# Performance work log

Measured on AMD Instinct MI355X. Metric: run time of the kernel, lower is better.

The kernel has to match this reference:

```python
import jax, jax.numpy as jnp
import numpy as np

DEPTH = 6            # full octree depth (64^3 effective resolution)
DATA_DIM = 28        # 9*3 SH coeffs + 1 density -> sh_order = 2
SH_ORDER = 2
B_RAYS = 32768
MAX_STEPS = 192      # max DDA cell crossings for a 64^3 grid
STEP_SIZE = 0.001
BG_BRIGHTNESS = 1.0

SH_C0 = 0.28209479177387814
SH_C1 = 0.4886025119029199
SH_C2 = (1.0925484305920792, -1.0925484305920792, 0.31539156525252005,
         -1.0925484305920792, 0.5462742152960396)


def _build_full_tree_child():
    # Full octree in BFS order; child stores relative offsets, 0 = leaf.
    n_nodes = (8 ** DEPTH - 1) // 7
    child = np.zeros((n_nodes, 2, 2, 2), np.int32)
    off = 0
    for d in range(DEPTH - 1):
        cnt = 8 ** d
        nxt = off + cnt
        r = np.arange(cnt)
        j = nxt + r[:, None] * 8 + np.arange(8)[None, :]
        child[off:nxt] = (j - (off + r)[:, None]).reshape(cnt, 2, 2, 2)
        off = nxt
    return child


def setup_inputs() -> dict:
    key = jax.random.key(0)
    k0, k1, k2, k3 = jax.random.split(key, 4)
    n_nodes = (8 ** DEPTH - 1) // 7
    data = jax.random.normal(k0, (n_nodes, 2, 2, 2, DATA_DIM), jnp.float32)
    child = jnp.asarray(_build_full_tree_child())
    origins = jax.random.normal(k1, (B_RAYS, 3), jnp.float32) * 0.3
    dirs = jax.random.normal(k2, (B_RAYS, 3), jnp.float32)
    vd = jax.random.normal(k3, (B_RAYS, 3), jnp.float32)
    viewdirs = vd / jnp.linalg.norm(vd, axis=-1, keepdims=True)
    offset = jnp.full((3,), 0.5, jnp.float32)
    invradius = jnp.full((1,), 0.5, jnp.float32)
    return dict(data=data, child=child, origins=origins, dirs=dirs,
                viewdirs=viewdirs, offset=offset, invradius=invradius)


def eval_sh_bases2(v):
    # svox sh.eval_sh_bases for order 2 -> (B, 9)
    x, y, z = v[:, 0], v[:, 1], v[:, 2]
    return jnp.stack([
        jnp.full_like(x, SH_C0),
        -SH_C1 * y, SH_C1 * z, -SH_C1 * x,
        SH_C2[0] * x * y, SH_C2[1] * y * z,
        SH_C2[2] * (2.0 * z * z - x * x - y * y),
        SH_C2[3] * x * z, SH_C2[4] * (x * x - y * y)], axis=-1)


def dda_unit(cen, invdir):
    # intersection of ray with the unit cube [0,1]^3; returns (tmin>=0, tmax)
    t1 = -cen * invdir
    t2 = t1 + invdir
    tmin = jnp.maximum(0.0, jnp.max(jnp.minimum(t1, t2), axis=-1))
    tmax = jnp.minimum(1e9, jnp.min(jnp.maximum(t1, t2), axis=-1))
    return tmin, tmax


def tree_query(data, child, pos):
    # Walk the octree from root; returns (leaf rgba (B,D), cell size (B,), cell corner (B,3))
    B = pos.shape[0]
    node = jnp.zeros((B,), jnp.int32)
    corner = jnp.zeros_like(pos)
    csz = jnp.ones((B,), pos.dtype)
    done = jnp.zeros((B,), bool)
    fin_node = node
    fin_idx = jnp.zeros((B, 3), jnp.int32)
    for _ in range(DEPTH):
        rel = (pos - corner) / csz[:, None]
        idx = jnp.clip(jnp.floor(rel * 2.0).astype(jnp.int32), 0, 1)
        c_cell = csz * 0.5
        corner_cell = corner + idx.astype(pos.dtype) * c_cell[:, None]
        ch = child[node, idx[:, 0], idx[:, 1], idx[:, 2]]
        leaf = ch == 0
        newly = (~done) & leaf
        fin_node = jnp.where(newly, node, fin_node)
        fin_idx = jnp.where(newly[:, None], idx, fin_idx)
        upd = ~done
        corner = jnp.where(upd[:, None], corner_cell, corner)
        csz = jnp.where(upd, c_cell, csz)
        node = jnp.where(upd & (~leaf), node + ch, node)
        done = done | leaf
    rgba = data[fin_node, fin_idx[:, 0], fin_idx[:, 1], fin_idx[:, 2]]
    return rgba, csz, corner


def _render(data, child, origins, dirs, viewdirs, offset, invradius):
    B = origins.shape[0]
    og = offset[None, :] + origins * invradius[0]          # world2tree
    d = dirs / jnp.linalg.norm(dirs, axis=-1, keepdims=True)
    invd = 1.0 / (d + 1e-9)
    t0, tmax = dda_unit(og, invd)
    sh_mult = eval_sh_bases2(viewdirs)                     # (B, 9)
    delta_scale = 1.0 / invradius[0]

    def body(carry, _):
        t, light, out, active = carry
        pos = og + t[:, None] * d
        rgba, csz, corner = tree_query(data, child, pos)
        pos_t = (pos - corner) / csz[:, None]
        tmn, tmx = dda_unit(pos_t, invd)
        dt = (tmx - tmn) * csz + STEP_SIZE
        att = jnp.exp(-dt * jax.nn.relu(rgba[:, -1]) * delta_scale)
        w = jnp.where(active, light * (1.0 - att), 0.0)
        rgb_sh = rgba[:, :-1].reshape(-1, 3, (SH_ORDER + 1) ** 2)
        rgb = jax.nn.sigmoid(jnp.sum(sh_mult[:, None, :] * rgb_sh, axis=-1))
        out = out + w[:, None] * rgb
        light = jnp.where(active, light * att, light)
        t = jnp.where(active, t + dt, t)
        active = active & (t < tmax)
        return (t, light, out, active), None

    init = (t0, jnp.ones((B,), og.dtype), jnp.zeros((B, 3), og.dtype), t0 < tmax)
    (t, light, out, active), _ = jax.lax.scan(body, init, None, length=MAX_STEPS)
    return out + BG_BRIGHTNESS * light[:, None]


_render_jit = jax.jit(_render)


def reference(data, child, origins, dirs, viewdirs, offset, invradius):
    return _render_jit(data, child, origins, dirs, viewdirs, offset, invradius)
```

## Files before the change

kernel.cpp:

```cpp
#include <hip/hip_runtime.h>
#include <hip/hip_fp16.h>
#include <math.h>

#pragma clang fp contract(off)


constexpr float STEP_SIZE  = 0.001f;
constexpr int   KC   = 16;
constexpr int   CH   = 12;
constexpr float SH_C0   = 0.28209479177387814f;
constexpr float SH_C1   = 0.4886025119029199f;
constexpr float SH_C2_0 = 1.0925484305920792f;
constexpr float SH_C2_1 = -1.0925484305920792f;
constexpr float SH_C2_2 = 0.31539156525252005f;
constexpr float SH_C2_3 = -1.0925484305920792f;
constexpr float SH_C2_4 = 0.5462742152960396f;
constexpr unsigned LEAF_BASE   = 37448u;
constexpr unsigned NLEAF       = 262144u;
constexpr unsigned LEAF_F32OFF = LEAF_BASE * 28u;
constexpr size_t   TABLE_BYTES = (size_t)NLEAF * 64;

__device__ __forceinline__ unsigned spread6(unsigned v) {
    v = (v | (v << 8)) & 0x0300F00Fu;
    v = (v | (v << 4)) & 0x030C30C3u;
    v = (v | (v << 2)) & 0x09249249u;
    return v;
}

__device__ __forceinline__ float2 h2f(unsigned u) {
    return __half22float2(__builtin_bit_cast(__half2, u));
}

__global__ void __launch_bounds__(256)
vr_convert(const float* __restrict__ data, __half2* __restrict__ o, int total)
{
    int tid = blockIdx.x * 256 + threadIdx.x;
    if (tid >= total) return;
    unsigned c = (unsigned)tid >> 4, j = (unsigned)tid & 15u;
    const float* src = data + LEAF_F32OFF + c * 28u;
    float a, b;
    if (j == 0u)      { a = src[27]; b = src[0]; }
    else if (j < 14u) { a = src[2 * j - 1]; b = src[2 * j]; }
    else              { a = 0.f; b = 0.f; }
    o[tid] = __float22half2_rn(make_float2(a, b));
}

#define RAY_SETUP                                                             \
    const float invr   = invradius[0];                                        \
    float ogx = offset[0] + origins[3 * ray + 0] * invr;                      \
    float ogy = offset[1] + origins[3 * ray + 1] * invr;                      \
    float ogz = offset[2] + origins[3 * ray + 2] * invr;                      \
    float Dx = dirs[3 * ray + 0], Dy = dirs[3 * ray + 1], Dz = dirs[3 * ray + 2]; \
    float dn = sqrtf(Dx * Dx + Dy * Dy + Dz * Dz);                            \
    float dx = Dx / dn, dy = Dy / dn, dz = Dz / dn;                           \
    float ivx = 1.0f / (dx + 1e-9f);                                          \
    float ivy = 1.0f / (dy + 1e-9f);                                          \
    float ivz = 1.0f / (dz + 1e-9f);                                          \
    float t1x = -ogx * ivx, t2x = t1x + ivx;                                  \
    float t1y = -ogy * ivy, t2y = t1y + ivy;                                  \
    float t1z = -ogz * ivz, t2z = t1z + ivz;                                  \
    float t    = fmaxf(0.f, fmaxf(fmaxf(fminf(t1x, t2x), fminf(t1y, t2y)),    \
                                  fminf(t1z, t2z)));                          \
    float tmax = fminf(1e9f, fminf(fminf(fmaxf(t1x, t2x), fmaxf(t1y, t2y)),   \
                                   fmaxf(t1z, t2z)));

#define GEO_BODY(OUT_DT, OUT_VOX)                                            \
    float px = ogx + t * dx;                                                 \
    float py = ogy + t * dy;                                                 \
    float pz = ogz + t * dz;                                                 \
    float fx = px * 64.f, fy = py * 64.f, fz = pz * 64.f;                    \
    float vxf = fminf(fmaxf(floorf(fx), 0.f), 63.f);                         \
    float vyf = fminf(fmaxf(floorf(fy), 0.f), 63.f);                         \
    float vzf = fminf(fmaxf(floorf(fz), 0.f), 63.f);                         \
    float ptx = fx - vxf, pty = fy - vyf, ptz = fz - vzf;                    \
    float b1x = -ptx * ivx, b2x = b1x + ivx;                                 \
    float b1y = -pty * ivy, b2y = b1y + ivy;                                 \
    float b1z = -ptz * ivz, b2z = b1z + ivz;                                 \
    float tmn = fmaxf(0.f, fmaxf(fmaxf(fminf(b1x, b2x), fminf(b1y, b2y)),    \
                                 fminf(b1z, b2z)));                          \
    float tmx = fminf(1e9f, fminf(fminf(fmaxf(b1x, b2x), fmaxf(b1y, b2y)),   \
                                  fmaxf(b1z, b2z)));                         \
    OUT_DT = (tmx - tmn) * 0.015625f + STEP_SIZE;                            \
    OUT_VOX = (spread6((unsigned)(int)vxf) << 2) |                           \
              (spread6((unsigned)(int)vyf) << 1) |                           \
               spread6((unsigned)(int)vzf);

__global__ void __launch_bounds__(64)
vr_tpass(const float* __restrict__ origins,
         const float* __restrict__ dirs,
         const float* __restrict__ offset,
         const float* __restrict__ invradius,
         float* __restrict__ tb, int nrays)
{
    int ray = blockIdx.x * 64 + threadIdx.x;
    if (ray >= nrays) return;
    RAY_SETUP
    bool act = t < tmax;
    for (int c = 0; c < KC; ++c) {
        tb[c * nrays + ray] = t;
        if (c == KC - 1) break;
        for (int s = 0; s < CH; ++s) {
            if (act) {
                float dtv; unsigned vox;
                GEO_BODY(dtv, vox)
                (void)vox;
                t += dtv;
                act = (t < tmax);
            }
        }
    }
}

__global__ void __launch_bounds__(64)
vr_march16(const uint4* __restrict__ table,
           const float* __restrict__ tb,
           const float* __restrict__ origins,
           const float* __restrict__ dirs,
           const float* __restrict__ viewdirs,
           const float* __restrict__ offset,
           const float* __restrict__ invradius,
           float4* __restrict__ ws4, int nrays)
{
    int ray = blockIdx.x * 64 + threadIdx.x;
    if (ray >= nrays) return;
    int chunk = blockIdx.y;

    RAY_SETUP
    const float dscale = 1.0f / invr;

    t = tb[chunk * nrays + ray];
    bool act = t < tmax;

    float lcl = 1.f, o0 = 0.f, o1 = 0.f, o2 = 0.f;

    if (__any(act)) {
        float vx_ = viewdirs[3 * ray + 0], vy_ = viewdirs[3 * ray + 1],
              vz_ = viewdirs[3 * ray + 2];
        float sh0 = SH_C0;
        float sh1 = -SH_C1 * vy_;
        float sh2 =  SH_C1 * vz_;
        float sh3 = -SH_C1 * vx_;
        float sh4 = SH_C2_0 * (vx_ * vy_);
        float sh5 = SH_C2_1 * (vy_ * vz_);
        float sh6 = SH_C2_2 * (2.f * (vz_ * vz_) - vx_ * vx_ - vy_ * vy_);
        float sh7 = SH_C2_3 * (vx_ * vz_);
        float sh8 = SH_C2_4 * (vx_ * vx_ - vy_ * vy_);

        for (int s = 0; s < CH; ++s) {
            if (!__any(act)) break;
            if (act) {
                float dtv; unsigned vox;
                GEO_BODY(dtv, vox)

                const uint4* tp = table + (size_t)vox * 4u;
                uint4 q0 = tp[0], q1 = tp[1], q2 = tp[2], q3 = tp[3];
                float2 F0 = h2f(q0.x);
                float sigma = F0.x;
                if (sigma > 0.f) {
                    float2 F1 = h2f(q0.y), F2 = h2f(q0.z), F3 = h2f(q0.w);
                    float2 F4 = h2f(q1.x), F5 = h2f(q1.y), F6 = h2f(q1.z), F7 = h2f(q1.w);
                    float2 F8 = h2f(q2.x), F9 = h2f(q2.y), F10 = h2f(q2.z), F11 = h2f(q2.w);
                    float2 F12 = h2f(q3.x), F13 = h2f(q3.y);

                    float d0 = fmaf(sh0, F0.y, fmaf(sh1, F1.x, fmaf(sh2, F1.y,
                               fmaf(sh3, F2.x, fmaf(sh4, F2.y, fmaf(sh5, F3.x,
                               fmaf(sh6, F3.y, fmaf(sh7, F4.x, sh8 * F4.y))))))));
                    float d1 = fmaf(sh0, F5.x, fmaf(sh1, F5.y, fmaf(sh2, F6.x,
                               fmaf(sh3, F6.y, fmaf(sh4, F7.x, fmaf(sh5, F7.y,
                               fmaf(sh6, F8.x, fmaf(sh7, F8.y, sh8 * F9.x))))))));
                    float d2 = fmaf(sh0, F9.y, fmaf(sh1, F10.x, fmaf(sh2, F10.y,
                               fmaf(sh3, F11.x, fmaf(sh4, F11.y, fmaf(sh5, F12.x,
                               fmaf(sh6, F12.y, fmaf(sh7, F13.x, sh8 * F13.y))))))));

                    float att = __expf(-dtv * sigma * dscale);
                    float w   = lcl * (1.f - att);
                    float s0  = __builtin_amdgcn_rcpf(1.f + __expf(-d0));
                    float s1  = __builtin_amdgcn_rcpf(1.f + __expf(-d1));
                    float s2  = __builtin_amdgcn_rcpf(1.f + __expf(-d2));
                    o0 = fmaf(w, s0, o0);
                    o1 = fmaf(w, s1, o1);
                    o2 = fmaf(w, s2, o2);
                    lcl *= att;
                }

                t += dtv;
                act = (t < tmax);
            }
        }
    }

    ws4[chunk * nrays + ray] = make_float4(o0, o1, o2, lcl);
}

__global__ void vr_march32(const float* __restrict__ data,
                           const float* __restrict__ origins,
                           const float* __restrict__ dirs,
                           const float* __restrict__ viewdirs,
                           const float* __restrict__ offset,
                           const float* __restrict__ invradius,
                           float4* __restrict__ ws4, int nrays)
{
    constexpr int CHS = 48;
    int ray = blockIdx.x * 64 + threadIdx.x;
    if (ray >= nrays) return;
    int chunk = blockIdx.y;

    RAY_SETUP
    const float dscale = 1.0f / invr;

    float vx_ = viewdirs[3 * ray + 0], vy_ = viewdirs[3 * ray + 1],
          vz_ = viewdirs[3 * ray + 2];
    float sh0 = SH_C0;
    float sh1 = -SH_C1 * vy_;
    float sh2 =  SH_C1 * vz_;
    float sh3 = -SH_C1 * vx_;
    float sh4 = SH_C2_0 * (vx_ * vy_);
    float sh5 = SH_C2_1 * (vy_ * vz_);
    float sh6 = SH_C2_2 * (2.f * (vz_ * vz_) - vx_ * vx_ - vy_ * vy_);
    float sh7 = SH_C2_3 * (vx_ * vz_);
    float sh8 = SH_C2_4 * (vx_ * vx_ - vy_ * vy_);

    float lcl = 1.f, o0 = 0.f, o1 = 0.f, o2 = 0.f;
    bool act = t < tmax;

    int warm = chunk * CHS;
    for (int s = 0; s < warm; ++s) {
        if (!__any(act)) break;
        if (act) {
            float dtv; unsigned vox;
            GEO_BODY(dtv, vox)
            (void)vox;
            t += dtv;
            act = (t < tmax);
        }
    }

    for (int s = 0; s < CHS; ++s) {
        if (!__any(act)) break;
        if (act) {
            float dtv; unsigned vox;
            GEO_BODY(dtv, vox)
            const float4* p = (const float4*)(data + (LEAF_BASE + vox) * 28u);
            float4 a0 = p[0], a1 = p[1], a2 = p[2], a3 = p[3],
                   a4 = p[4], a5 = p[5], a6 = p[6];
            float d0 = fmaf(sh0, a0.x, fmaf(sh1, a0.y, fmaf(sh2, a0.z,
                       fmaf(sh3, a0.w, fmaf(sh4, a1.x, fmaf(sh5, a1.y,
                       fmaf(sh6, a1.z, fmaf(sh7, a1.w, sh8 * a2.x))))))));
            float d1 = fmaf(sh0, a2.y, fmaf(sh1, a2.z, fmaf(sh2, a2.w,
                       fmaf(sh3, a3.x, fmaf(sh4, a3.y, fmaf(sh5, a3.z,
                       fmaf(sh6, a3.w, fmaf(sh7, a4.x, sh8 * a4.y))))))));
            float d2 = fmaf(sh0, a4.z, fmaf(sh1, a4.w, fmaf(sh2, a5.x,
                       fmaf(sh3, a5.y, fmaf(sh4, a5.z, fmaf(sh5, a5.w,
                       fmaf(sh6, a6.x, fmaf(sh7, a6.y, sh8 * a6.z))))))));
            float att = __expf(-dtv * fmaxf(a6.w, 0.f) * dscale);
            float w   = lcl * (1.f - att);
            float s0  = __builtin_amdgcn_rcpf(1.f + __expf(-d0));
            float s1  = __builtin_amdgcn_rcpf(1.f + __expf(-d1));
            float s2  = __builtin_amdgcn_rcpf(1.f + __expf(-d2));
            o0 = fmaf(w, s0, o0);
            o1 = fmaf(w, s1, o1);
            o2 = fmaf(w, s2, o2);
            lcl *= att;
            t += dtv;
            act = (t < tmax);
        }
    }

    ws4[chunk * nrays + ray] = make_float4(o0, o1, o2, lcl);
}

template<int K>
__global__ void __launch_bounds__(256)
vr_combine(const float4* __restrict__ ws4, float* __restrict__ out, int nrays)
{
    int r = blockIdx.x * 256 + threadIdx.x;
    if (r >= nrays) return;
    float4 c = ws4[(K - 1) * nrays + r];
    float ax = c.x, ay = c.y, az = c.z, L = c.w;
#pragma unroll
    for (int cidx = K - 2; cidx >= 0; --cidx) {
        float4 p = ws4[cidx * nrays + r];
        ax = p.x + p.w * ax;
        ay = p.y + p.w * ay;
        az = p.z + p.w * az;
        L *= p.w;
    }
    out[3 * r + 0] = ax + L;
    out[3 * r + 1] = ay + L;
    out[3 * r + 2] = az + L;
}

extern "C" void kernel_launch(void* const* d_in, const int* in_sizes, int n_in,
                              void* d_out, int out_size, void* d_ws, size_t ws_size,
                              hipStream_t stream)
{
    const float* data      = (const float*)d_in[0];
    const float* origins   = (const float*)d_in[2];
    const float* dirs      = (const float*)d_in[3];
    const float* viewdirs  = (const float*)d_in[4];
    const float* offset    = (const float*)d_in[5];
    const float* invradius = (const float*)d_in[6];
    float* out = (float*)d_out;

    int nrays = in_sizes[2] / 3;
    size_t tb_bytes   = (size_t)KC * nrays * sizeof(float);
    size_t part_bytes = (size_t)KC * nrays * sizeof(float4);
    dim3 gridC((nrays + 255) / 256), blockC(256);

    if (ws_size >= TABLE_BYTES + tb_bytes + part_bytes) {
        __half2* table_h2 = (__half2*)d_ws;
        float*   tb       = (float*)((char*)d_ws + TABLE_BYTES);
        float4*  ws4      = (float4*)((char*)d_ws + TABLE_BYTES + tb_bytes);

        int total = (int)(NLEAF * 16u);
        dim3 gridV((total + 255) / 256), blockV(256);
        hipLaunchKernelGGL(vr_convert, gridV, blockV, 0, stream,
                           data, table_h2, total);

        dim3 gridT((nrays + 63) / 64), blockT(64);
        hipLaunchKernelGGL(vr_tpass, gridT, blockT, 0, stream,
                           origins, dirs, offset, invradius, tb, nrays);

        dim3 gridM((nrays + 63) / 64, KC), blockM(64);
        hipLaunchKernelGGL(vr_march16, gridM, blockM, 0, stream,
                           (const uint4*)d_ws, tb, origins, dirs, viewdirs,
                           offset, invradius, ws4, nrays);

        hipLaunchKernelGGL((vr_combine<KC>), gridC, blockC, 0, stream,
                           ws4, out, nrays);
    } else {
        float4* ws4 = (float4*)d_ws;
        dim3 gridM((nrays + 63) / 64, 4), blockM(64);
        hipLaunchKernelGGL(vr_march32, gridM, blockM, 0, stream,
                           data, origins, dirs, viewdirs,
                           offset, invradius, ws4, nrays);
        hipLaunchKernelGGL((vr_combine<4>), gridC, blockC, 0, stream,
                           ws4, out, nrays);
    }
}
```

Before: 57.34 us.

## Split leaf table into sigma/color halves, batch lookups, drop t-pass kernel

The fp16 leaf table is split into an 8-byte part holding sigma plus the first coefficients and a 48-byte part holding the rest of the color data. The march kernel now prefetches the small part for batches of 8 steps before shading, and loads the large part only when sigma is positive. The separate t-pass kernel is removed: each chunk re-marches its warm-up steps itself, with fewer, longer chunks (8x24 instead of 16x12). This trades repeated geometry work in later chunks for one less launch and one less global buffer, and aims to hide gather latency and skip color loads for empty cells.

```diff
diff --git a/kernel.cpp b/kernel.cpp
--- a/kernel.cpp
+++ b/kernel.cpp
@@ -6,8 +6,9 @@
 
 
 constexpr float STEP_SIZE  = 0.001f;
-constexpr int   KC   = 16;
-constexpr int   CH   = 12;
+constexpr int   KC   = 8;
+constexpr int   CH   = 24;
+constexpr int   SB   = 8;
 constexpr float SH_C0   = 0.28209479177387814f;
 constexpr float SH_C1   = 0.4886025119029199f;
 constexpr float SH_C2_0 = 1.0925484305920792f;
@@ -18,7 +19,8 @@
 constexpr unsigned LEAF_BASE   = 37448u;
 constexpr unsigned NLEAF       = 262144u;
 constexpr unsigned LEAF_F32OFF = LEAF_BASE * 28u;
-constexpr size_t   TABLE_BYTES = (size_t)NLEAF * 64;
+constexpr size_t   A_BYTES = (size_t)NLEAF * 8;
+constexpr size_t   B_BYTES = (size_t)NLEAF * 48;
 
 __device__ __forceinline__ unsigned spread6(unsigned v) {
     v = (v | (v << 8)) & 0x0300F00Fu;
@@ -30,19 +32,27 @@
 __device__ __forceinline__ float2 h2f(unsigned u) {
     return __half22float2(__builtin_bit_cast(__half2, u));
 }
+__device__ __forceinline__ unsigned f2h2(float a, float b) {
+    return __builtin_bit_cast(unsigned, __float22half2_rn(make_float2(a, b)));
+}
 
 __global__ void __launch_bounds__(256)
-vr_convert(const float* __restrict__ data, __half2* __restrict__ o, int total)
-{
-    int tid = blockIdx.x * 256 + threadIdx.x;
-    if (tid >= total) return;
-    unsigned c = (unsigned)tid >> 4, j = (unsigned)tid & 15u;
-    const float* src = data + LEAF_F32OFF + c * 28u;
-    float a, b;
-    if (j == 0u)      { a = src[27]; b = src[0]; }
-    else if (j < 14u) { a = src[2 * j - 1]; b = src[2 * j]; }
-    else              { a = 0.f; b = 0.f; }
-    o[tid] = __float22half2_rn(make_float2(a, b));
+vr_convert(const float* __restrict__ data,
+           uint2* __restrict__ tabA, uint4* __restrict__ tabB)
+{
+    unsigned leaf = blockIdx.x * 256 + threadIdx.x;
+    if (leaf >= NLEAF) return;
+    const float4* sp = (const float4*)(data + LEAF_F32OFF + leaf * 28u);
+    float4 a0 = sp[0], a1 = sp[1], a2 = sp[2], a3 = sp[3],
+           a4 = sp[4], a5 = sp[5], a6 = sp[6];
+    tabA[leaf] = make_uint2(f2h2(a6.w, a0.x), f2h2(a0.y, a0.z));
+    uint4* bp = tabB + (size_t)leaf * 3u;
+    bp[0] = make_uint4(f2h2(a0.w, a1.x), f2h2(a1.y, a1.z),
+                       f2h2(a1.w, a2.x), f2h2(a2.y, a2.z));
+    bp[1] = make_uint4(f2h2(a2.w, a3.x), f2h2(a3.y, a3.z),
+                       f2h2(a3.w, a4.x), f2h2(a4.y, a4.z));
+    bp[2] = make_uint4(f2h2(a4.w, a5.x), f2h2(a5.y, a5.z),
+                       f2h2(a5.w, a6.x), f2h2(a6.y, a6.z));
 }
 
 #define RAY_SETUP                                                             \
@@ -63,6 +73,19 @@
                                   fminf(t1z, t2z)));                          \
     float tmax = fminf(1e9f, fminf(fminf(fmaxf(t1x, t2x), fmaxf(t1y, t2y)),   \
                                    fmaxf(t1z, t2z)));
+
+#define SH_SETUP                                                              \
+    float vx_ = viewdirs[3 * ray + 0], vy_ = viewdirs[3 * ray + 1],           \
+          vz_ = viewdirs[3 * ray + 2];                                        \
+    float sh0 = SH_C0;                                                        \
+    float sh1 = -SH_C1 * vy_;                                                 \
+    float sh2 =  SH_C1 * vz_;                                                 \
+    float sh3 = -SH_C1 * vx_;                                                 \
+    float sh4 = SH_C2_0 * (vx_ * vy_);                                        \
+    float sh5 = SH_C2_1 * (vy_ * vz_);                                        \
+    float sh6 = SH_C2_2 * (2.f * (vz_ * vz_) - vx_ * vx_ - vy_ * vy_);        \
+    float sh7 = SH_C2_3 * (vx_ * vz_);                                        \
+    float sh8 = SH_C2_4 * (vx_ * vx_ - vy_ * vy_);
 
 #define GEO_BODY(OUT_DT, OUT_VOX)                                            \
     float px = ogx + t * dx;                                                 \
@@ -85,94 +108,84 @@
               (spread6((unsigned)(int)vyf) << 1) |                           \
                spread6((unsigned)(int)vzf);
 
-__global__ void __launch_bounds__(64)
-vr_tpass(const float* __restrict__ origins,
-         const float* __restrict__ dirs,
-         const float* __restrict__ offset,
-         const float* __restrict__ invradius,
-         float* __restrict__ tb, int nrays)
+__global__ void vr_march16(const uint2* __restrict__ tabA,
+                           const uint4* __restrict__ tabB,
+                           const float* __restrict__ origins,
+                           const float* __restrict__ dirs,
+                           const float* __restrict__ viewdirs,
+                           const float* __restrict__ offset,
+                           const float* __restrict__ invradius,
+                           float4* __restrict__ ws4, int nrays)
 {
     int ray = blockIdx.x * 64 + threadIdx.x;
     if (ray >= nrays) return;
+    int chunk = blockIdx.y;
+
     RAY_SETUP
+    const float dscale = 1.0f / invr;
+    SH_SETUP
+
+    float lcl = 1.f, o0 = 0.f, o1 = 0.f, o2 = 0.f;
     bool act = t < tmax;
-    for (int c = 0; c < KC; ++c) {
-        tb[c * nrays + ray] = t;
-        if (c == KC - 1) break;
-        for (int s = 0; s < CH; ++s) {
+
+    int warm = chunk * CH;
+    for (int s = 0; s < warm; ++s) {
+        if (!__any(act)) break;
+        if (act) {
+            float dtv; unsigned vox;
+            GEO_BODY(dtv, vox)
+            (void)vox;
+            t += dtv;
+            act = (t < tmax);
+        }
+    }
+
+    for (int b = 0; b < CH / SB; ++b) {
+        if (!__any(act)) break;
+
+        float    dtA[SB];
+        unsigned voxA[SB];
+        uint2    qA[SB];
+        unsigned amask = 0u;
+
+#pragma unroll
+        for (int j = 0; j < SB; ++j) {
             if (act) {
                 float dtv; unsigned vox;
                 GEO_BODY(dtv, vox)
-                (void)vox;
+                dtA[j]  = dtv;
+                voxA[j] = vox;
+                qA[j]   = tabA[vox];
+                amask  |= (1u << j);
                 t += dtv;
                 act = (t < tmax);
             }
         }
-    }
-}
-
-__global__ void __launch_bounds__(64)
-vr_march16(const uint4* __restrict__ table,
-           const float* __restrict__ tb,
-           const float* __restrict__ origins,
-           const float* __restrict__ dirs,
-           const float* __restrict__ viewdirs,
-           const float* __restrict__ offset,
-           const float* __restrict__ invradius,
-           float4* __restrict__ ws4, int nrays)
-{
-    int ray = blockIdx.x * 64 + threadIdx.x;
-    if (ray >= nrays) return;
-    int chunk = blockIdx.y;
-
-    RAY_SETUP
-    const float dscale = 1.0f / invr;
-
-    t = tb[chunk * nrays + ray];
-    bool act = t < tmax;
-
-    float lcl = 1.f, o0 = 0.f, o1 = 0.f, o2 = 0.f;
-
-    if (__any(act)) {
-        float vx_ = viewdirs[3 * ray + 0], vy_ = viewdirs[3 * ray + 1],
-              vz_ = viewdirs[3 * ray + 2];
-        float sh0 = SH_C0;
-        float sh1 = -SH_C1 * vy_;
-        float sh2 =  SH_C1 * vz_;
-        float sh3 = -SH_C1 * vx_;
-        float sh4 = SH_C2_0 * (vx_ * vy_);
-        float sh5 = SH_C2_1 * (vy_ * vz_);
-        float sh6 = SH_C2_2 * (2.f * (vz_ * vz_) - vx_ * vx_ - vy_ * vy_);
-        float sh7 = SH_C2_3 * (vx_ * vz_);
-        float sh8 = SH_C2_4 * (vx_ * vx_ - vy_ * vy_);
-
-        for (int s = 0; s < CH; ++s) {
-            if (!__any(act)) break;
-            if (act) {
-                float dtv; unsigned vox;
-                GEO_BODY(dtv, vox)
-
-                const uint4* tp = table + (size_t)vox * 4u;
-                uint4 q0 = tp[0], q1 = tp[1], q2 = tp[2], q3 = tp[3];
-                float2 F0 = h2f(q0.x);
+
+#pragma unroll
+        for (int j = 0; j < SB; ++j) {
+            if ((amask >> j) & 1u) {
+                float2 F0 = h2f(qA[j].x);
                 float sigma = F0.x;
                 if (sigma > 0.f) {
-                    float2 F1 = h2f(q0.y), F2 = h2f(q0.z), F3 = h2f(q0.w);
-                    float2 F4 = h2f(q1.x), F5 = h2f(q1.y), F6 = h2f(q1.z), F7 = h2f(q1.w);
-                    float2 F8 = h2f(q2.x), F9 = h2f(q2.y), F10 = h2f(q2.z), F11 = h2f(q2.w);
-                    float2 F12 = h2f(q3.x), F13 = h2f(q3.y);
+                    float2 F1 = h2f(qA[j].y);
+                    const uint4* bp = tabB + (size_t)voxA[j] * 3u;
+                    uint4 B0 = bp[0], B1 = bp[1], B2 = bp[2];
+                    float2 G0 = h2f(B0.x), G1 = h2f(B0.y), G2 = h2f(B0.z), G3 = h2f(B0.w);
+                    float2 H0 = h2f(B1.x), H1 = h2f(B1.y), H2 = h2f(B1.z), H3 = h2f(B1.w);
+                    float2 I0 = h2f(B2.x), I1 = h2f(B2.y), I2 = h2f(B2.z), I3 = h2f(B2.w);
 
                     float d0 = fmaf(sh0, F0.y, fmaf(sh1, F1.x, fmaf(sh2, F1.y,
-                               fmaf(sh3, F2.x, fmaf(sh4, F2.y, fmaf(sh5, F3.x,
-                               fmaf(sh6, F3.y, fmaf(sh7, F4.x, sh8 * F4.y))))))));
-                    float d1 = fmaf(sh0, F5.x, fmaf(sh1, F5.y, fmaf(sh2, F6.x,
-                               fmaf(sh3, F6.y, fmaf(sh4, F7.x, fmaf(sh5, F7.y,
-                               fmaf(sh6, F8.x, fmaf(sh7, F8.y, sh8 * F9.x))))))));
-                    float d2 = fmaf(sh0, F9.y, fmaf(sh1, F10.x, fmaf(sh2, F10.y,
-                               fmaf(sh3, F11.x, fmaf(sh4, F11.y, fmaf(sh5, F12.x,
-                               fmaf(sh6, F12.y, fmaf(sh7, F13.x, sh8 * F13.y))))))));
-
-                    float att = __expf(-dtv * sigma * dscale);
+                               fmaf(sh3, G0.x, fmaf(sh4, G0.y, fmaf(sh5, G1.x,
+                               fmaf(sh6, G1.y, fmaf(sh7, G2.x, sh8 * G2.y))))))));
+                    float d1 = fmaf(sh0, G3.x, fmaf(sh1, G3.y, fmaf(sh2, H0.x,
+                               fmaf(sh3, H0.y, fmaf(sh4, H1.x, fmaf(sh5, H1.y,
+                               fmaf(sh6, H2.x, fmaf(sh7, H2.y, sh8 * H3.x))))))));
+                    float d2 = fmaf(sh0, H3.y, fmaf(sh1, I0.x, fmaf(sh2, I0.y,
+                               fmaf(sh3, I1.x, fmaf(sh4, I1.y, fmaf(sh5, I2.x,
+                               fmaf(sh6, I2.y, fmaf(sh7, I3.x, sh8 * I3.y))))))));
+
+                    float att = __expf(-dtA[j] * sigma * dscale);
                     float w   = lcl * (1.f - att);
                     float s0  = __builtin_amdgcn_rcpf(1.f + __expf(-d0));
                     float s1  = __builtin_amdgcn_rcpf(1.f + __expf(-d1));
@@ -182,9 +195,6 @@
                     o2 = fmaf(w, s2, o2);
                     lcl *= att;
                 }
-
-                t += dtv;
-                act = (t < tmax);
             }
         }
     }
@@ -207,18 +217,7 @@
 
     RAY_SETUP
     const float dscale = 1.0f / invr;
-
-    float vx_ = viewdirs[3 * ray + 0], vy_ = viewdirs[3 * ray + 1],
-          vz_ = viewdirs[3 * ray + 2];
-    float sh0 = SH_C0;
-    float sh1 = -SH_C1 * vy_;
-    float sh2 =  SH_C1 * vz_;
-    float sh3 = -SH_C1 * vx_;
-    float sh4 = SH_C2_0 * (vx_ * vy_);
-    float sh5 = SH_C2_1 * (vy_ * vz_);
-    float sh6 = SH_C2_2 * (2.f * (vz_ * vz_) - vx_ * vx_ - vy_ * vy_);
-    float sh7 = SH_C2_3 * (vx_ * vz_);
-    float sh8 = SH_C2_4 * (vx_ * vx_ - vy_ * vy_);
+    SH_SETUP
 
     float lcl = 1.f, o0 = 0.f, o1 = 0.f, o2 = 0.f;
     bool act = t < tmax;
@@ -303,27 +302,21 @@
     float* out = (float*)d_out;
 
     int nrays = in_sizes[2] / 3;
-    size_t tb_bytes   = (size_t)KC * nrays * sizeof(float);
     size_t part_bytes = (size_t)KC * nrays * sizeof(float4);
     dim3 gridC((nrays + 255) / 256), blockC(256);
 
-    if (ws_size >= TABLE_BYTES + tb_bytes + part_bytes) {
-        __half2* table_h2 = (__half2*)d_ws;
-        float*   tb       = (float*)((char*)d_ws + TABLE_BYTES);
-        float4*  ws4      = (float4*)((char*)d_ws + TABLE_BYTES + tb_bytes);
-
-        int total = (int)(NLEAF * 16u);
-        dim3 gridV((total + 255) / 256), blockV(256);
+    if (ws_size >= A_BYTES + B_BYTES + part_bytes) {
+        uint2*  tabA = (uint2*)d_ws;
+        uint4*  tabB = (uint4*)((char*)d_ws + A_BYTES);
+        float4* ws4  = (float4*)((char*)d_ws + A_BYTES + B_BYTES);
+
+        dim3 gridV((NLEAF + 255) / 256), blockV(256);
         hipLaunchKernelGGL(vr_convert, gridV, blockV, 0, stream,
-                           data, table_h2, total);
-
-        dim3 gridT((nrays + 63) / 64), blockT(64);
-        hipLaunchKernelGGL(vr_tpass, gridT, blockT, 0, stream,
-                           origins, dirs, offset, invradius, tb, nrays);
+                           data, tabA, tabB);
 
         dim3 gridM((nrays + 63) / 64, KC), blockM(64);
         hipLaunchKernelGGL(vr_march16, gridM, blockM, 0, stream,
-                           (const uint4*)d_ws, tb, origins, dirs, viewdirs,
+                           tabA, tabB, origins, dirs, viewdirs,
                            offset, invradius, ws4, nrays);
 
         hipLaunchKernelGGL((vr_combine<KC>), gridC, blockC, 0, stream,
```

New measurement: 49.45 us, median of 2. 13.8% less time.
